# Kernel tuning notes

Measured on AMD Instinct MI355X. Metric: run time of the kernel, lower is better.

Reference implementation:

```python
import jax, jax.numpy as jnp
import numpy as np

N_BLOCKS = 16
BLOCK = 512  # filters per conv layer
N = N_BLOCKS * BLOCK  # 8192 total nodes (filters)
E = 128  # embedding_feature_len
LAYER_NUM = 2
NEG = -9e15  # matches -9000000000000000.0 zero_vec


def _build_adj():
    filter_num = [BLOCK] * N_BLOCKS
    adj = np.zeros((N, N), dtype=np.float32)
    row = last = filter_num[0]
    for num in filter_num:
        adj[row:row + num, row - last:row] = 1.0
        row += num
        last = num
    np.fill_diagonal(adj, 0.0)
    return adj


def setup_inputs() -> dict:
    key = jax.random.key(0)
    k_h, k_w0, k_w1 = jax.random.split(key, 3)
    h = jax.random.normal(k_h, (N, E), dtype=jnp.float32)
    adj = jnp.asarray(_build_adj())
    s = 1.0 / np.sqrt(E)
    W0 = jax.random.normal(k_w0, (E, E), dtype=jnp.float32) * s
    b0 = jnp.zeros((E,), dtype=jnp.float32)
    W1 = jax.random.normal(k_w1, (E, E), dtype=jnp.float32) * s
    b1 = jnp.zeros((E,), dtype=jnp.float32)
    return {"h": h, "adj": adj, "W0": W0, "b0": b0, "W1": W1, "b1": b1}


def _gat_layer(h, adj, W, b):
    n, e = h.shape
    # attention = h @ h.T / sqrt(E)
    att = jnp.matmul(h, h.T) / jnp.sqrt(jnp.asarray(e, h.dtype))
    A = jnp.where(adj > 0, att, jnp.asarray(NEG, h.dtype))
    A = jax.nn.softmax(A, axis=1)
    # A = (A + I) / 2, without materializing a dense NxN eye
    d = jnp.arange(n)
    A = A * 0.5
    A = A.at[d, d].add(0.5)
    # rows [:num_filter_1layer] overridden with identity rows
    nf1 = jnp.sum(adj[:, 0] != 0)
    mask = d < nf1  # [N]
    A = jnp.where(mask[:, None], 0.0, A)
    A = A.at[d, d].set(jnp.where(mask, 1.0, A[d, d]))
    h_new = jnp.matmul(h, W.T) + b  # nn.Linear
    return jax.nn.relu(jnp.matmul(A, h_new))


def reference(h, adj, W0, b0, W1, b1):
    x = _gat_layer(h, adj, W0, b0)
    x = _gat_layer(x, adj, W1, b1)
    return x
```

## Files before the change

### kernel.cpp

```cpp
#include <hip/hip_runtime.h>

typedef __attribute__((ext_vector_type(4))) float f32x4;
typedef __attribute__((ext_vector_type(8))) short s16x8;
typedef unsigned int u32;
typedef __attribute__((ext_vector_type(2))) u32 u32x2;
typedef __attribute__((ext_vector_type(4))) u32 u32x4;

#define NN 8192
#define EE 128
#define SCLOG2E 0.12751743f

__device__ __forceinline__ ushort f2bf(float f){
  u32 u = __builtin_bit_cast(u32, f);
  u += 0x7fffu + ((u >> 16) & 1u);
  return (ushort)(u >> 16);
}
__device__ __forceinline__ float bf2f(ushort h){
  u32 u = ((u32)h) << 16;
  return __builtin_bit_cast(float, u);
}
__device__ __forceinline__ void gload16(const void* g, void* l){
  __builtin_amdgcn_global_load_lds((const __attribute__((address_space(1))) u32*)g,
                                   (__attribute__((address_space(3))) u32*)l, 16, 0, 0);
}
#define VM_WAIT0   do{ asm volatile("s_waitcnt vmcnt(0)" ::: "memory"); __builtin_amdgcn_sched_barrier(0);}while(0)
#define LGKM_WAIT0 do{ asm volatile("s_waitcnt lgkmcnt(0)" ::: "memory"); __builtin_amdgcn_sched_barrier(0);}while(0)
#define CODE_FENCE do{ asm volatile("" ::: "memory"); __builtin_amdgcn_sched_barrier(0);}while(0)

template<int LAYER>
__global__ __launch_bounds__(256, 1) void gat_k(
    const float*  __restrict__ hf,
    const ushort* __restrict__ Xbf,
    const float*  __restrict__ Wf, const float* __restrict__ bias,
    ushort* __restrict__ Ybf,
    float*  __restrict__ Yf)
{
  __shared__ __align__(16) char smem[74240];
  const int t = threadIdx.x;
  const int wv = t >> 6, l = t & 63, lr = l & 15, lg = l >> 4;
  const int wid = ((blockIdx.x & 7) << 5) | (blockIdx.x >> 3);
  const u32 chkoff = wv*8192;
  char* PB = smem + 65536 + wv*2048;
  float* Ls = (float*)(smem + 73728);
  char* AG = smem + 65536;

  const int idx = wid - 16;
  const int rb = (wid < 16) ? wid*32 : 512 + (idx>>4)*512 + (idx&15)*32;
  s16x8 af[2][4];

  s16x8 wfrag[2][4];
  if constexpr (LAYER == 2){
    #pragma unroll
    for (int ntl=0;ntl<2;++ntl)
      #pragma unroll
      for (int kb=0;kb<4;++kb){
        f32x4 w0 = *(const f32x4*)&Wf[(wv*32 + ntl*16 + lr)*EE + kb*32 + lg*8];
        f32x4 w1 = *(const f32x4*)&Wf[(wv*32 + ntl*16 + lr)*EE + kb*32 + lg*8 + 4];
        #pragma unroll
        for (int j=0;j<4;++j){ wfrag[ntl][kb][j] = (short)f2bf(w0[j]); wfrag[ntl][kb][j+4] = (short)f2bf(w1[j]); }
      }
  }

  if (wid >= 16){
    const int pbase = (idx >> 4) * 512;

    s16x8 qh[2][4];
    #pragma unroll
    for (int h2=0;h2<2;++h2)
      #pragma unroll
      for (int kb=0;kb<4;++kb){
        if constexpr (LAYER == 1){
          f32x4 a0 = *(const f32x4*)&hf[(rb+h2*16+lr)*EE + kb*32 + lg*8];
          f32x4 a1 = *(const f32x4*)&hf[(rb+h2*16+lr)*EE + kb*32 + lg*8 + 4];
          #pragma unroll
          for (int j=0;j<4;++j){
            qh[h2][kb][j]   = (short)f2bf(a0[j]);
            qh[h2][kb][j+4] = (short)f2bf(a1[j]);
          }
        } else {
          qh[h2][kb] = *(const s16x8*)&Xbf[(rb+h2*16+lr)*EE + kb*32 + lg*8];
        }
      }

    const int srow = (l>>3)*4 + ((l&7)>>1);
    const int scol = (l&1)*8;

    const ushort* srcrow2 = (LAYER == 2) ? &Xbf[srow*EE + scol] : nullptr;
    auto stage2 = [&](int c){
      const ushort* src = srcrow2 + (pbase + c*32)*EE;
      #pragma unroll
      for (int it=0; it<8; ++it)
        gload16(src + it*16, smem + chkoff + it*1024);
    };

    const float* srcrow1 = (LAYER == 1) ? &hf[srow*EE + scol] : nullptr;
    f32x4 stg[8][2];
    auto ldissue = [&](int c){
      const float* src = srcrow1 + (pbase + c*32)*EE;
      #pragma unroll
      for (int it=0; it<8; ++it){
        stg[it][0] = *(const f32x4*)(src + it*16);
        stg[it][1] = *(const f32x4*)(src + it*16 + 4);
      }
    };
    auto cvwrite = [&](){
      #pragma unroll
      for (int it=0; it<8; ++it){
        u32x4 pk;
        pk[0] = (u32)f2bf(stg[it][0][0]) | ((u32)f2bf(stg[it][0][1]) << 16);
        pk[1] = (u32)f2bf(stg[it][0][2]) | ((u32)f2bf(stg[it][0][3]) << 16);
        pk[2] = (u32)f2bf(stg[it][1][0]) | ((u32)f2bf(stg[it][1][1]) << 16);
        pk[3] = (u32)f2bf(stg[it][1][2]) | ((u32)f2bf(stg[it][1][3]) << 16);
        *(u32x4*)(smem + chkoff + it*1024 + l*16) = pk;
      }
    };

    f32x4 O[2][8];
    #pragma unroll
    for (int h2=0;h2<2;++h2)
      #pragma unroll
      for (int nt=0;nt<8;++nt) O[h2][nt] = (f32x4){0.f,0.f,0.f,0.f};
    float lsum[2][4] = {{0.f,0.f,0.f,0.f},{0.f,0.f,0.f,0.f}};

    const u32 trbase = chkoff + (u32)((l>>4)*256 + (l&15)*8);
    const u32 pfbase = (u32)(65536 + wv*2048 + lg*256 + lr*8);

    if constexpr (LAYER == 1){
      ldissue(wv*4);
      cvwrite();
      ldissue(wv*4 + 1);
      CODE_FENCE;
    } else {
      stage2(wv*4);
    }

    for (int tc=0; tc<4; ++tc){
      if constexpr (LAYER == 2) VM_WAIT0;

      s16x8 kf[2][4];
      #pragma unroll
      for (int pt=0;pt<2;++pt)
        #pragma unroll
        for (int kb=0;kb<4;++kb)
          kf[pt][kb] = *(const s16x8*)(smem + chkoff + (kb*2+(lg>>1))*1024
                         + (pt*4 + (lr>>2))*128 + (lr&3)*32 + (lg&1)*16);

      s16x8 vf[8];
      #pragma unroll
      for (int nt=0;nt<8;++nt){
        u32x2 a, b;
        u32 off = trbase + (u32)(nt*1024);
        asm volatile("ds_read_b64_tr_b16 %0, %2\n\t"
                     "ds_read_b64_tr_b16 %1, %2 offset:128"
                     : "=&v"(a), "=&v"(b) : "v"(off));
        u32x4 c4; c4[0]=a[0]; c4[1]=a[1]; c4[2]=b[0]; c4[3]=b[1];
        vf[nt] = __builtin_bit_cast(s16x8, c4);
      }
      LGKM_WAIT0;

      if constexpr (LAYER == 1){
        if (tc < 3){
          cvwrite();
          if (tc < 2) ldissue(wv*4 + tc + 2);
          CODE_FENCE;
        }
      } else {
        if (tc < 3) stage2(wv*4 + tc + 1);
      }

      f32x4 sv[2][2];
      __builtin_amdgcn_s_setprio(1);
      #pragma unroll
      for (int h2=0;h2<2;++h2)
        #pragma unroll
        for (int pt=0;pt<2;++pt){
          f32x4 s = (f32x4){0.f,0.f,0.f,0.f};
          #pragma unroll
          for (int kb=0;kb<4;++kb)
            s = __builtin_amdgcn_mfma_f32_16x16x32_bf16(qh[h2][kb], kf[pt][kb], s, 0,0,0);
          sv[h2][pt] = s;
        }
      __builtin_amdgcn_s_setprio(0);

      #pragma unroll
      for (int h2=0;h2<2;++h2)
        #pragma unroll
        for (int r=0;r<4;++r){
          float e0 = __builtin_amdgcn_exp2f(sv[h2][0][r]*SCLOG2E);
          float e1 = __builtin_amdgcn_exp2f(sv[h2][1][r]*SCLOG2E);
          sv[h2][0][r] = e0; sv[h2][1][r] = e1;
          lsum[h2][r] += e0 + e1;
        }
      #pragma unroll
      for (int h2=0;h2<2;++h2)
        #pragma unroll
        for (int pt=0;pt<2;++pt){
          u32x2 pk;
          pk[0] = (u32)f2bf(sv[h2][pt][0]) | ((u32)f2bf(sv[h2][pt][1]) << 16);
          pk[1] = (u32)f2bf(sv[h2][pt][2]) | ((u32)f2bf(sv[h2][pt][3]) << 16);
          *(u32x2*)(PB + h2*1024 + (lr + pt*16)*32 + lg*8) = pk;
        }
      s16x8 pf[2];
      #pragma unroll
      for (int h2=0;h2<2;++h2){
        u32x2 a, b;
        u32 off = pfbase + (u32)(h2*1024);
        asm volatile("ds_read_b64_tr_b16 %0, %2\n\t"
                     "ds_read_b64_tr_b16 %1, %2 offset:128"
                     : "=&v"(a), "=&v"(b) : "v"(off) : "memory");
        u32x4 c4; c4[0]=a[0]; c4[1]=a[1]; c4[2]=b[0]; c4[3]=b[1];
        pf[h2] = __builtin_bit_cast(s16x8, c4);
      }
      LGKM_WAIT0;
      __builtin_amdgcn_s_setprio(1);
      #pragma unroll
      for (int h2=0;h2<2;++h2)
        #pragma unroll
        for (int nt=0;nt<8;++nt)
          O[h2][nt] = __builtin_amdgcn_mfma_f32_16x16x32_bf16(pf[h2], vf[nt], O[h2][nt], 0,0,0);
      __builtin_amdgcn_s_setprio(0);
    }

    float qcv[2][2][4];
    #pragma unroll
    for (int h2=0;h2<2;++h2)
      #pragma unroll
      for (int ntl=0;ntl<2;++ntl){
        int col = (wv*2 + ntl)*16 + lr;
        #pragma unroll
        for (int r=0;r<4;++r){
          int row = rb + h2*16 + lg*4 + r;
          if constexpr (LAYER == 1) qcv[h2][ntl][r] = hf[row*EE + col];
          else                      qcv[h2][ntl][r] = bf2f(Xbf[row*EE + col]);
        }
      }

    #pragma unroll
    for (int h2=0;h2<2;++h2)
      #pragma unroll
      for (int r=0;r<4;++r){
        float s = lsum[h2][r];
        #pragma unroll
        for (int off=1; off<16; off<<=1) s += __shfl_xor(s, off, 16);
        lsum[h2][r] = s;
      }
    #pragma unroll
    for (int h2=0;h2<2;++h2)
      #pragma unroll
      for (int nt=0;nt<8;++nt)
        *(f32x4*)(smem + h2*32768 + wv*8192 + nt*1024 + l*16) = O[h2][nt];
    if (lr == 0){
      #pragma unroll
      for (int h2=0;h2<2;++h2)
        #pragma unroll
        for (int r=0;r<4;++r) Ls[h2*64 + wv*16 + lg*4 + r] = lsum[h2][r];
    }
    __syncthreads();

    f32x4 om[2][2][4];
    #pragma unroll
    for (int h2=0;h2<2;++h2)
      #pragma unroll
      for (int ntl=0;ntl<2;++ntl){
        int nt = wv*2 + ntl;
        #pragma unroll
        for (int r2=0;r2<4;++r2)
          om[h2][ntl][r2] = *(const f32x4*)(smem + h2*32768 + r2*8192 + nt*1024 + l*16);
      }
    float Li[2][4];
    #pragma unroll
    for (int h2=0;h2<2;++h2)
      #pragma unroll
      for (int r=0;r<4;++r){
        int q = lg*4 + r;
        Li[h2][r] = __builtin_amdgcn_rcpf(Ls[h2*64+q] + Ls[h2*64+16+q] + Ls[h2*64+32+q] + Ls[h2*64+48+q]);
      }
    __syncthreads();

    #pragma unroll
    for (int h2=0;h2<2;++h2)
      #pragma unroll
      for (int ntl=0;ntl<2;++ntl){
        int nt = wv*2 + ntl;
        int col = nt*16 + lr;
        #pragma unroll
        for (int r=0;r<4;++r){
          float s4 = om[h2][ntl][0][r]+om[h2][ntl][1][r]+om[h2][ntl][2][r]+om[h2][ntl][3][r];
          float agg = 0.5f*qcv[h2][ntl][r] + 0.5f*(s4 * Li[h2][r]);
          int q = h2*16 + lg*4 + r;
          *(ushort*)(AG + q*256 + (((col>>3) ^ (q&7))*16) + (col&7)*2) = f2bf(agg);
        }
      }
    __syncthreads();
    #pragma unroll
    for (int h2=0;h2<2;++h2)
      #pragma unroll
      for (int kb=0;kb<4;++kb)
        af[h2][kb] = *(const s16x8*)(AG + (h2*16+lr)*256 + (((kb*4+lg) ^ (lr&7))*16));
  } else {
    #pragma unroll
    for (int h2=0;h2<2;++h2)
      #pragma unroll
      for (int kb=0;kb<4;++kb){
        if constexpr (LAYER == 1){
          f32x4 a0 = *(const f32x4*)&hf[(rb+h2*16+lr)*EE + kb*32 + lg*8];
          f32x4 a1 = *(const f32x4*)&hf[(rb+h2*16+lr)*EE + kb*32 + lg*8 + 4];
          #pragma unroll
          for (int j=0;j<4;++j){
            af[h2][kb][j]   = (short)f2bf(a0[j]);
            af[h2][kb][j+4] = (short)f2bf(a1[j]);
          }
        } else {
          af[h2][kb] = *(const s16x8*)&Xbf[(rb + h2*16 + lr)*EE + kb*32 + lg*8];
        }
      }
  }

  f32x4 acc[2][2];
  #pragma unroll
  for (int h2=0;h2<2;++h2){ acc[h2][0]=(f32x4){0.f,0.f,0.f,0.f}; acc[h2][1]=(f32x4){0.f,0.f,0.f,0.f}; }
  #pragma unroll
  for (int ntl=0;ntl<2;++ntl)
    #pragma unroll
    for (int kb=0;kb<4;++kb){
      s16x8 wb;
      if constexpr (LAYER == 2){
        wb = wfrag[ntl][kb];
      } else {
        f32x4 w0 = *(const f32x4*)&Wf[(wv*32 + ntl*16 + lr)*EE + kb*32 + lg*8];
        f32x4 w1 = *(const f32x4*)&Wf[(wv*32 + ntl*16 + lr)*EE + kb*32 + lg*8 + 4];
        #pragma unroll
        for (int j=0;j<4;++j){ wb[j] = (short)f2bf(w0[j]); wb[j+4] = (short)f2bf(w1[j]); }
      }
      #pragma unroll
      for (int h2=0;h2<2;++h2)
        acc[h2][ntl] = __builtin_amdgcn_mfma_f32_16x16x32_bf16(af[h2][kb], wb, acc[h2][ntl], 0,0,0);
    }
  #pragma unroll
  for (int h2=0;h2<2;++h2)
    #pragma unroll
    for (int ntl=0;ntl<2;++ntl){
      int col = wv*32 + ntl*16 + lr;
      float bv = bias[col];
      #pragma unroll
      for (int r=0;r<4;++r){
        int row = rb + h2*16 + lg*4 + r;
        float v = fmaxf(acc[h2][ntl][r] + bv, 0.f);
        if constexpr (LAYER == 1) Ybf[row*EE + col] = f2bf(v);
        else                      Yf[row*EE + col] = v;
      }
    }
}

extern "C" void kernel_launch(void* const* d_in, const int* in_sizes, int n_in,
                              void* d_out, int out_size, void* d_ws, size_t ws_size,
                              hipStream_t stream) {
  const float* h  = (const float*)d_in[0];
  const float* W0 = (const float*)d_in[2];
  const float* b0 = (const float*)d_in[3];
  const float* W1 = (const float*)d_in[4];
  const float* b1 = (const float*)d_in[5];
  float* out = (float*)d_out;

  ushort* X1hi = (ushort*)d_ws;

  gat_k<1><<<256, 256, 0, stream>>>(h, nullptr, W0, b0, X1hi, nullptr);
  gat_k<2><<<256, 256, 0, stream>>>(nullptr, X1hi, W1, b1, nullptr, out);
}
```

Measured before the change: 28.23 us.

## Halve rows per block and double grid for two blocks per CU

Each block now processes 16 query rows instead of 32. This halves the register accumulators and the LDS footprint, doubles the grid to 512 blocks, and raises launch bounds to allow two blocks per CU. The aim is more resident waves to hide memory and LDS latency and to fill more CUs. In exchange, the key/value chunks of a 512-node predecessor block are reloaded and converted twice as often per output row, and MFMA reuse of each K/V fragment is halved.

After: 35.26 us. 1.25x slower.

```diff
diff --git a/kernel.cpp b/kernel.cpp
--- a/kernel.cpp
+++ b/kernel.cpp
@@ -28,25 +28,26 @@
 #define CODE_FENCE do{ asm volatile("" ::: "memory"); __builtin_amdgcn_sched_barrier(0);}while(0)
 
 template<int LAYER>
-__global__ __launch_bounds__(256, 1) void gat_k(
+__global__ __launch_bounds__(256, 2) void gat_k(
     const float*  __restrict__ hf,
     const ushort* __restrict__ Xbf,
     const float*  __restrict__ Wf, const float* __restrict__ bias,
     ushort* __restrict__ Ybf,
     float*  __restrict__ Yf)
 {
-  __shared__ __align__(16) char smem[74240];
+  __shared__ __align__(16) char smem[37120];
   const int t = threadIdx.x;
   const int wv = t >> 6, l = t & 63, lr = l & 15, lg = l >> 4;
-  const int wid = ((blockIdx.x & 7) << 5) | (blockIdx.x >> 3);
+  const int bid = blockIdx.x;
+  const int wid = ((bid & 7) << 6) | (bid >> 3);
   const u32 chkoff = wv*8192;
-  char* PB = smem + 65536 + wv*2048;
-  float* Ls = (float*)(smem + 73728);
-  char* AG = smem + 65536;
-
-  const int idx = wid - 16;
-  const int rb = (wid < 16) ? wid*32 : 512 + (idx>>4)*512 + (idx&15)*32;
-  s16x8 af[2][4];
+  char* PB = smem + 32768 + wv*1024;
+  float* Ls = (float*)(smem + 36864);
+  char* AG = smem + 32768;
+
+  const int idx = wid - 32;
+  const int rb = (wid < 32) ? wid*16 : 512 + (idx>>5)*512 + (idx&31)*16;
+  s16x8 af[4];
 
   s16x8 wfrag[2][4];
   if constexpr (LAYER == 2){
@@ -61,26 +62,24 @@
       }
   }
 
-  if (wid >= 16){
-    const int pbase = (idx >> 4) * 512;
-
-    s16x8 qh[2][4];
-    #pragma unroll
-    for (int h2=0;h2<2;++h2)
-      #pragma unroll
-      for (int kb=0;kb<4;++kb){
-        if constexpr (LAYER == 1){
-          f32x4 a0 = *(const f32x4*)&hf[(rb+h2*16+lr)*EE + kb*32 + lg*8];
-          f32x4 a1 = *(const f32x4*)&hf[(rb+h2*16+lr)*EE + kb*32 + lg*8 + 4];
-          #pragma unroll
-          for (int j=0;j<4;++j){
-            qh[h2][kb][j]   = (short)f2bf(a0[j]);
-            qh[h2][kb][j+4] = (short)f2bf(a1[j]);
-          }
-        } else {
-          qh[h2][kb] = *(const s16x8*)&Xbf[(rb+h2*16+lr)*EE + kb*32 + lg*8];
+  if (wid >= 32){
+    const int pbase = (idx >> 5) * 512;
+
+    s16x8 qh[4];
+    #pragma unroll
+    for (int kb=0;kb<4;++kb){
+      if constexpr (LAYER == 1){
+        f32x4 a0 = *(const f32x4*)&hf[(rb+lr)*EE + kb*32 + lg*8];
+        f32x4 a1 = *(const f32x4*)&hf[(rb+lr)*EE + kb*32 + lg*8 + 4];
+        #pragma unroll
+        for (int j=0;j<4;++j){
+          qh[kb][j]   = (short)f2bf(a0[j]);
+          qh[kb][j+4] = (short)f2bf(a1[j]);
         }
-      }
+      } else {
+        qh[kb] = *(const s16x8*)&Xbf[(rb+lr)*EE + kb*32 + lg*8];
+      }
+    }
 
     const int srow = (l>>3)*4 + ((l&7)>>1);
     const int scol = (l&1)*8;
@@ -115,15 +114,13 @@
       }
     };
 
-    f32x4 O[2][8];
-    #pragma unroll
-    for (int h2=0;h2<2;++h2)
-      #pragma unroll
-      for (int nt=0;nt<8;++nt) O[h2][nt] = (f32x4){0.f,0.f,0.f,0.f};
-    float lsum[2][4] = {{0.f,0.f,0.f,0.f},{0.f,0.f,0.f,0.f}};
+    f32x4 O[8];
+    #pragma unroll
+    for (int nt=0;nt<8;++nt) O[nt] = (f32x4){0.f,0.f,0.f,0.f};
+    float lsum[4] = {0.f,0.f,0.f,0.f};
 
     const u32 trbase = chkoff + (u32)((l>>4)*256 + (l&15)*8);
-    const u32 pfbase = (u32)(65536 + wv*2048 + lg*256 + lr*8);
+    const u32 pfbase = (u32)(32768 + wv*1024 + lg*256 + lr*8);
 
     if constexpr (LAYER == 1){
       ldissue(wv*4);
@@ -168,157 +165,129 @@
         if (tc < 3) stage2(wv*4 + tc + 1);
       }
 
-      f32x4 sv[2][2];
+      f32x4 sv[2];
       __builtin_amdgcn_s_setprio(1);
       #pragma unroll
-      for (int h2=0;h2<2;++h2)
-        #pragma unroll
-        for (int pt=0;pt<2;++pt){
-          f32x4 s = (f32x4){0.f,0.f,0.f,0.f};
-          #pragma unroll
-          for (int kb=0;kb<4;++kb)
-            s = __builtin_amdgcn_mfma_f32_16x16x32_bf16(qh[h2][kb], kf[pt][kb], s, 0,0,0);
-          sv[h2][pt] = s;
-        }
+      for (int pt=0;pt<2;++pt){
+        f32x4 s = (f32x4){0.f,0.f,0.f,0.f};
+        #pragma unroll
+        for (int kb=0;kb<4;++kb)
+          s = __builtin_amdgcn_mfma_f32_16x16x32_bf16(qh[kb], kf[pt][kb], s, 0,0,0);
+        sv[pt] = s;
+      }
       __builtin_amdgcn_s_setprio(0);
 
       #pragma unroll
-      for (int h2=0;h2<2;++h2)
-        #pragma unroll
-        for (int r=0;r<4;++r){
-          float e0 = __builtin_amdgcn_exp2f(sv[h2][0][r]*SCLOG2E);
-          float e1 = __builtin_amdgcn_exp2f(sv[h2][1][r]*SCLOG2E);
-          sv[h2][0][r] = e0; sv[h2][1][r] = e1;
-          lsum[h2][r] += e0 + e1;
-        }
-      #pragma unroll
-      for (int h2=0;h2<2;++h2)
-        #pragma unroll
-        for (int pt=0;pt<2;++pt){
-          u32x2 pk;
-          pk[0] = (u32)f2bf(sv[h2][pt][0]) | ((u32)f2bf(sv[h2][pt][1]) << 16);
-          pk[1] = (u32)f2bf(sv[h2][pt][2]) | ((u32)f2bf(sv[h2][pt][3]) << 16);
-          *(u32x2*)(PB + h2*1024 + (lr + pt*16)*32 + lg*8) = pk;
-        }
-      s16x8 pf[2];
-      #pragma unroll
-      for (int h2=0;h2<2;++h2){
+      for (int r=0;r<4;++r){
+        float e0 = __builtin_amdgcn_exp2f(sv[0][r]*SCLOG2E);
+        float e1 = __builtin_amdgcn_exp2f(sv[1][r]*SCLOG2E);
+        sv[0][r] = e0; sv[1][r] = e1;
+        lsum[r] += e0 + e1;
+      }
+      #pragma unroll
+      for (int pt=0;pt<2;++pt){
+        u32x2 pk;
+        pk[0] = (u32)f2bf(sv[pt][0]) | ((u32)f2bf(sv[pt][1]) << 16);
+        pk[1] = (u32)f2bf(sv[pt][2]) | ((u32)f2bf(sv[pt][3]) << 16);
+        *(u32x2*)(PB + (lr + pt*16)*32 + lg*8) = pk;
+      }
+      s16x8 pf;
+      {
         u32x2 a, b;
-        u32 off = pfbase + (u32)(h2*1024);
         asm volatile("ds_read_b64_tr_b16 %0, %2\n\t"
                      "ds_read_b64_tr_b16 %1, %2 offset:128"
-                     : "=&v"(a), "=&v"(b) : "v"(off) : "memory");
+                     : "=&v"(a), "=&v"(b) : "v"(pfbase) : "memory");
         u32x4 c4; c4[0]=a[0]; c4[1]=a[1]; c4[2]=b[0]; c4[3]=b[1];
-        pf[h2] = __builtin_bit_cast(s16x8, c4);
+        pf = __builtin_bit_cast(s16x8, c4);
       }
       LGKM_WAIT0;
       __builtin_amdgcn_s_setprio(1);
       #pragma unroll
-      for (int h2=0;h2<2;++h2)
-        #pragma unroll
-        for (int nt=0;nt<8;++nt)
-          O[h2][nt] = __builtin_amdgcn_mfma_f32_16x16x32_bf16(pf[h2], vf[nt], O[h2][nt], 0,0,0);
+      for (int nt=0;nt<8;++nt)
+        O[nt] = __builtin_amdgcn_mfma_f32_16x16x32_bf16(pf, vf[nt], O[nt], 0,0,0);
       __builtin_amdgcn_s_setprio(0);
     }
 
-    float qcv[2][2][4];
-    #pragma unroll
-    for (int h2=0;h2<2;++h2)
-      #pragma unroll
-      for (int ntl=0;ntl<2;++ntl){
-        int col = (wv*2 + ntl)*16 + lr;
-        #pragma unroll
-        for (int r=0;r<4;++r){
-          int row = rb + h2*16 + lg*4 + r;
-          if constexpr (LAYER == 1) qcv[h2][ntl][r] = hf[row*EE + col];
-          else                      qcv[h2][ntl][r] = bf2f(Xbf[row*EE + col]);
+    float qcv[2][4];
+    #pragma unroll
+    for (int ntl=0;ntl<2;++ntl){
+      int col = (wv*2 + ntl)*16 + lr;
+      #pragma unroll
+      for (int r=0;r<4;++r){
+        int row = rb + lg*4 + r;
+        if constexpr (LAYER == 1) qcv[ntl][r] = hf[row*EE + col];
+        else                      qcv[ntl][r] = bf2f(Xbf[row*EE + col]);
+      }
+    }
+
+    #pragma unroll
+    for (int r=0;r<4;++r){
+      float s = lsum[r];
+      #pragma unroll
+      for (int off=1; off<16; off<<=1) s += __shfl_xor(s, off, 16);
+      lsum[r] = s;
+    }
+    #pragma unroll
+    for (int nt=0;nt<8;++nt)
+      *(f32x4*)(smem + wv*8192 + nt*1024 + l*16) = O[nt];
+    if (lr == 0){
+      #pragma unroll
+      for (int r=0;r<4;++r) Ls[wv*16 + lg*4 + r] = lsum[r];
+    }
+    __syncthreads();
+
+    f32x4 om[2][4];
+    #pragma unroll
+    for (int ntl=0;ntl<2;++ntl){
+      int nt = wv*2 + ntl;
+      #pragma unroll
+      for (int w2=0;w2<4;++w2)
+        om[ntl][w2] = *(const f32x4*)(smem + w2*8192 + nt*1024 + l*16);
+    }
+    float Li[4];
+    #pragma unroll
+    for (int r=0;r<4;++r){
+      int q = lg*4 + r;
+      Li[r] = __builtin_amdgcn_rcpf(Ls[q] + Ls[16+q] + Ls[32+q] + Ls[48+q]);
+    }
+    __syncthreads();
+
+    #pragma unroll
+    for (int ntl=0;ntl<2;++ntl){
+      int nt = wv*2 + ntl;
+      int col = nt*16 + lr;
+      #pragma unroll
+      for (int r=0;r<4;++r){
+        float s4 = om[ntl][0][r]+om[ntl][1][r]+om[ntl][2][r]+om[ntl][3][r];
+        float agg = 0.5f*qcv[ntl][r] + 0.5f*(s4 * Li[r]);
+        int q = lg*4 + r;
+        *(ushort*)(AG + q*256 + (((col>>3) ^ (q&7))*16) + (col&7)*2) = f2bf(agg);
+      }
+    }
+    __syncthreads();
+    #pragma unroll
+    for (int kb=0;kb<4;++kb)
+      af[kb] = *(const s16x8*)(AG + lr*256 + (((kb*4+lg) ^ (lr&7))*16));
+  } else {
+    #pragma unroll
+    for (int kb=0;kb<4;++kb){
+      if constexpr (LAYER == 1){
+        f32x4 a0 = *(const f32x4*)&hf[(rb+lr)*EE + kb*32 + lg*8];
+        f32x4 a1 = *(const f32x4*)&hf[(rb+lr)*EE + kb*32 + lg*8 + 4];
+        #pragma unroll
+        for (int j=0;j<4;++j){
+          af[kb][j]   = (short)f2bf(a0[j]);
+          af[kb][j+4] = (short)f2bf(a1[j]);
         }
-      }
-
-    #pragma unroll
-    for (int h2=0;h2<2;++h2)
-      #pragma unroll
-      for (int r=0;r<4;++r){
-        float s = lsum[h2][r];
-        #pragma unroll
-        for (int off=1; off<16; off<<=1) s += __shfl_xor(s, off, 16);
-        lsum[h2][r] = s;
-      }
-    #pragma unroll
-    for (int h2=0;h2<2;++h2)
-      #pragma unroll
-      for (int nt=0;nt<8;++nt)
-        *(f32x4*)(smem + h2*32768 + wv*8192 + nt*1024 + l*16) = O[h2][nt];
-    if (lr == 0){
-      #pragma unroll
-      for (int h2=0;h2<2;++h2)
-        #pragma unroll
-        for (int r=0;r<4;++r) Ls[h2*64 + wv*16 + lg*4 + r] = lsum[h2][r];
-    }
-    __syncthreads();
-
-    f32x4 om[2][2][4];
-    #pragma unroll
-    for (int h2=0;h2<2;++h2)
-      #pragma unroll
-      for (int ntl=0;ntl<2;++ntl){
-        int nt = wv*2 + ntl;
-        #pragma unroll
-        for (int r2=0;r2<4;++r2)
-          om[h2][ntl][r2] = *(const f32x4*)(smem + h2*32768 + r2*8192 + nt*1024 + l*16);
-      }
-    float Li[2][4];
-    #pragma unroll
-    for (int h2=0;h2<2;++h2)
-      #pragma unroll
-      for (int r=0;r<4;++r){
-        int q = lg*4 + r;
-        Li[h2][r] = __builtin_amdgcn_rcpf(Ls[h2*64+q] + Ls[h2*64+16+q] + Ls[h2*64+32+q] + Ls[h2*64+48+q]);
-      }
-    __syncthreads();
-
-    #pragma unroll
-    for (int h2=0;h2<2;++h2)
-      #pragma unroll
-      for (int ntl=0;ntl<2;++ntl){
-        int nt = wv*2 + ntl;
-        int col = nt*16 + lr;
-        #pragma unroll
-        for (int r=0;r<4;++r){
-          float s4 = om[h2][ntl][0][r]+om[h2][ntl][1][r]+om[h2][ntl][2][r]+om[h2][ntl][3][r];
-          float agg = 0.5f*qcv[h2][ntl][r] + 0.5f*(s4 * Li[h2][r]);
-          int q = h2*16 + lg*4 + r;
-          *(ushort*)(AG + q*256 + (((col>>3) ^ (q&7))*16) + (col&7)*2) = f2bf(agg);
-        }
-      }
-    __syncthreads();
-    #pragma unroll
-    for (int h2=0;h2<2;++h2)
-      #pragma unroll
-      for (int kb=0;kb<4;++kb)
-        af[h2][kb] = *(const s16x8*)(AG + (h2*16+lr)*256 + (((kb*4+lg) ^ (lr&7))*16));
-  } else {
-    #pragma unroll
-    for (int h2=0;h2<2;++h2)
-      #pragma unroll
-      for (int kb=0;kb<4;++kb){
-        if constexpr (LAYER == 1){
-          f32x4 a0 = *(const f32x4*)&hf[(rb+h2*16+lr)*EE + kb*32 + lg*8];
-          f32x4 a1 = *(const f32x4*)&hf[(rb+h2*16+lr)*EE + kb*32 + lg*8 + 4];
-          #pragma unroll
-          for (int j=0;j<4;++j){
-            af[h2][kb][j]   = (short)f2bf(a0[j]);
-            af[h2][kb][j+4] = (short)f2bf(a1[j]);
-          }
-        } else {
-          af[h2][kb] = *(const s16x8*)&Xbf[(rb + h2*16 + lr)*EE + kb*32 + lg*8];
-        }
-      }
+      } else {
+        af[kb] = *(const s16x8*)&Xbf[(rb + lr)*EE + kb*32 + lg*8];
+      }
+    }
   }
 
-  f32x4 acc[2][2];
-  #pragma unroll
-  for (int h2=0;h2<2;++h2){ acc[h2][0]=(f32x4){0.f,0.f,0.f,0.f}; acc[h2][1]=(f32x4){0.f,0.f,0.f,0.f}; }
+  f32x4 acc[2];
+  acc[0] = (f32x4){0.f,0.f,0.f,0.f};
+  acc[1] = (f32x4){0.f,0.f,0.f,0.f};
   #pragma unroll
   for (int ntl=0;ntl<2;++ntl)
     #pragma unroll
@@ -332,24 +301,20 @@
         #pragma unroll
         for (int j=0;j<4;++j){ wb[j] = (short)f2bf(w0[j]); wb[j+4] = (short)f2bf(w1[j]); }
       }
-      #pragma unroll
-      for (int h2=0;h2<2;++h2)
-        acc[h2][ntl] = __builtin_amdgcn_mfma_f32_16x16x32_bf16(af[h2][kb], wb, acc[h2][ntl], 0,0,0);
+      acc[ntl] = __builtin_amdgcn_mfma_f32_16x16x32_bf16(af[kb], wb, acc[ntl], 0,0,0);
     }
   #pragma unroll
-  for (int h2=0;h2<2;++h2)
-    #pragma unroll
-    for (int ntl=0;ntl<2;++ntl){
-      int col = wv*32 + ntl*16 + lr;
-      float bv = bias[col];
-      #pragma unroll
-      for (int r=0;r<4;++r){
-        int row = rb + h2*16 + lg*4 + r;
-        float v = fmaxf(acc[h2][ntl][r] + bv, 0.f);
-        if constexpr (LAYER == 1) Ybf[row*EE + col] = f2bf(v);
-        else                      Yf[row*EE + col] = v;
-      }
-    }
+  for (int ntl=0;ntl<2;++ntl){
+    int col = wv*32 + ntl*16 + lr;
+    float bv = bias[col];
+    #pragma unroll
+    for (int r=0;r<4;++r){
+      int row = rb + lg*4 + r;
+      float v = fmaxf(acc[ntl][r] + bv, 0.f);
+      if constexpr (LAYER == 1) Ybf[row*EE + col] = f2bf(v);
+      else                      Yf[row*EE + col] = v;
+    }
+  }
 }
 
 extern "C" void kernel_launch(void* const* d_in, const int* in_sizes, int n_in,
@@ -364,6 +329,6 @@
 
   ushort* X1hi = (ushort*)d_ws;
 
-  gat_k<1><<<256, 256, 0, stream>>>(h, nullptr, W0, b0, X1hi, nullptr);
-  gat_k<2><<<256, 256, 0, stream>>>(nullptr, X1hi, W1, b1, nullptr, out);
-}
+  gat_k<1><<<512, 256, 0, stream>>>(h, nullptr, W0, b0, X1hi, nullptr);
+  gat_k<2><<<512, 256, 0, stream>>>(nullptr, X1hi, W1, b1, nullptr, out);
+}
```
